# Optimization experiments

Measured on AMD Instinct MI355X. Metric: run time of the kernel, lower is better.

## Reference

```python
import jax, jax.numpy as jnp
import numpy as np

B, N, NC = 16, 25200, 80          # batch, raw predictions, classes (COCO)
CONF_THRES = 0.25
IOU_THRES = 0.45
MAX_CAND = 1000                    # candidates kept after score top-k (pre-NMS)
CLS_OFFSET = 4096.0                # class-wise box offset (non-agnostic NMS trick)
EPS = 1e-7


def setup_inputs() -> dict:
    key = jax.random.key(0)
    # raw head output: [x, y, w, h, obj, cls0..cls79], values in [0,1]
    pred = jax.random.uniform(key, (B, N, 5 + NC), dtype=jnp.float32)
    return {"pred": pred}


def _xywh2xyxy(x):
    xy, wh = x[..., :2], x[..., 2:4]
    return jnp.concatenate([xy - wh * 0.5, xy + wh * 0.5], axis=-1)


def _box_iou(boxes):
    # boxes: [C, 4] xyxy -> pairwise IoU [C, C]
    area = (boxes[:, 2] - boxes[:, 0]) * (boxes[:, 3] - boxes[:, 1])
    lt = jnp.maximum(boxes[:, None, :2], boxes[None, :, :2])
    rb = jnp.minimum(boxes[:, None, 2:], boxes[None, :, 2:])
    wh = jnp.clip(rb - lt, 0.0)
    inter = wh[..., 0] * wh[..., 1]
    return inter / (area[:, None] + area[None, :] - inter + EPS)


def _nms_single(p):
    # p: [N, 5+NC] -> (out [MAX_CAND, 6] xyxy/conf/cls zero-padded, keep [MAX_CAND] bool)
    obj = p[:, 4]
    cls_scores = p[:, 5:] * obj[:, None]          # conf = obj * cls
    conf = jnp.max(cls_scores, axis=-1)
    cls_idx = jnp.argmax(cls_scores, axis=-1)
    valid = (obj > CONF_THRES) & (conf > CONF_THRES)
    score = jnp.where(valid, conf, -1.0)

    # pre-NMS top-k by score (sorted descending) — fixed-shape stand-in for boolean filter
    top_scores, idx = jax.lax.top_k(score, MAX_CAND)
    boxes = _xywh2xyxy(p[idx, :4])                # [C, 4]
    kconf = conf[idx]
    kcls = cls_idx[idx].astype(jnp.float32)
    valid_c = top_scores > 0.0

    # class-offset boxes so different classes never overlap (agnostic=False)
    off_boxes = boxes + kcls[:, None] * CLS_OFFSET
    iou = _box_iou(off_boxes)                     # [C, C]

    ar = jnp.arange(MAX_CAND)

    def body(i, keep):
        sup = keep[i] & (iou[i] > IOU_THRES) & (ar > i)
        return keep & jnp.logical_not(sup)

    keep = jax.lax.fori_loop(0, MAX_CAND, body, valid_c)

    out = jnp.concatenate([boxes, kconf[:, None], kcls[:, None]], axis=-1)  # [C, 6]
    out = jnp.where(keep[:, None], out, 0.0)
    return out, keep


def reference(pred):
    out, keep = jax.vmap(_nms_single)(pred)
    return out, keep
```

## Files before the change

### kernel.cpp

```cpp
#include <hip/hip_runtime.h>
#include <stdint.h>

typedef unsigned int u32;
typedef unsigned long long u64;

#define BATCH 16
#define NANCH 25200
#define NCLS 80
#define ROWF 85
#define MAXC 1000
#define CONF_T 0.25f
#define IOU_T 0.45f
#define EPS_F 1e-7f
#define TILE 64
#define NTILES ((NANCH + TILE - 1) / TILE)

__device__ __forceinline__ float iou_ref(float4 a, float4 b) {
#pragma clang fp contract(off)
  float ai = (a.z - a.x) * (a.w - a.y);
  float aj = (b.z - b.x) * (b.w - b.y);
  float ltx = fmaxf(a.x, b.x), lty = fmaxf(a.y, b.y);
  float rbx = fminf(a.z, b.z), rby = fminf(a.w, b.w);
  float wx = fmaxf(rbx - ltx, 0.0f), wy = fmaxf(rby - lty, 0.0f);
  float inter = wx * wy;
  return inter / (ai + aj - inter + EPS_F);
}

__global__ __launch_bounds__(256) void k1_score(const float* __restrict__ pred,
                                                u64* __restrict__ keys,
                                                u32* __restrict__ hist) {
  __shared__ float srow[TILE * ROWF];
  __shared__ u64 skeys[TILE];
  __shared__ u32 lh[256];
  int tid = threadIdx.x;
  int b = blockIdx.y;
  int t0 = blockIdx.x * TILE;
  int ntile = (t0 + TILE <= NANCH) ? TILE : (NANCH - t0);
  int nf4 = (ntile * ROWF) >> 2;

  lh[tid] = 0;
  const float4* src4 = (const float4*)(pred + ((size_t)b * NANCH + t0) * ROWF);
  float4* smem4 = (float4*)srow;
#pragma unroll
  for (int k = 0; k < 6; ++k) {
    int i = k * 256 + tid;
    if (i < nf4) smem4[i] = src4[i];
  }
  __syncthreads();

  int a = tid >> 2;
  int q = tid & 3;
  float best = -1e30f;
  int bidx = 0;
  float obj = 0.0f;
  if (a < ntile) {
    const float* row = srow + a * ROWF;
    obj = row[4];
    int c0 = q * 20;
#pragma unroll
    for (int c = 0; c < 20; ++c) {
      float s = row[5 + c0 + c] * obj;
      if (s > best) { best = s; bidx = c0 + c; }
    }
  }
#pragma unroll
  for (int off = 1; off < 4; off <<= 1) {
    float ob = __shfl_xor(best, off);
    int oi = __shfl_xor(bidx, off);
    if (ob > best || (ob == best && oi < bidx)) { best = ob; bidx = oi; }
  }
  if (q == 0 && a < ntile) {
    int n = t0 + a;
    bool valid = (obj > CONF_T) && (best > CONF_T);
    u32 hi;
    if (valid) hi = __float_as_uint(best) | 0x80000000u;
    else hi = ((u32)n * 2654435761u) >> 1;
    u32 lo = ((u32)(32767 - n) << 7) | (u32)bidx;
    skeys[a] = ((u64)hi << 32) | lo;
    atomicAdd(&lh[hi >> 24], 1u);
  }
  __syncthreads();
  if (tid < ntile) keys[(size_t)b * NANCH + t0 + tid] = skeys[tid];
  u32 v = lh[tid];
  if (v) atomicAdd(&hist[b * 256 + tid], v);
}

__global__ __launch_bounds__(1024) void k2_select(const float* __restrict__ pred,
                                                  const u64* __restrict__ keys,
                                                  const u32* __restrict__ hist,
                                                  float* __restrict__ selbox,
                                                  float* __restrict__ offbox,
                                                  float* __restrict__ selconf,
                                                  float* __restrict__ selcls,
                                                  u32* __restrict__ selvalid) {
  int b = blockIdx.x;
  int tid = threadIdx.x;
  int wv = tid >> 6, lane = tid & 63;
  __shared__ u32 h4[4096];
  __shared__ u32 wsum[16];
  __shared__ u32 sh_sel;
  __shared__ int sh_rank;
  __shared__ u32 scount;
  __shared__ u64 skey[2048];

  const u64* kb = keys + (size_t)b * NANCH;

  if (tid < 256) h4[tid] = hist[b * 256 + tid];
  __syncthreads();
  if (tid < 64) {
    int l = tid;
    u32 a0 = h4[4 * l], a1 = h4[4 * l + 1], a2 = h4[4 * l + 2], a3 = h4[4 * l + 3];
    u32 lsum = a0 + a1 + a2 + a3;
    u32 suf = lsum;
#pragma unroll
    for (int off = 1; off < 64; off <<= 1) {
      u32 tv = __shfl_down(suf, off);
      if (l + off < 64) suf += tv;
    }
    int rank = MAXC;
    u32 e3 = suf - lsum; u32 i3 = e3 + a3;
    u32 e2 = i3;         u32 i2 = e2 + a2;
    u32 e1 = i2;         u32 i1 = e1 + a1;
    u32 e0 = i1;         u32 i0 = e0 + a0;
    if ((int)i3 >= rank && (int)e3 < rank) { sh_sel = 4u*l+3u; sh_rank = rank-(int)e3; }
    if ((int)i2 >= rank && (int)e2 < rank) { sh_sel = 4u*l+2u; sh_rank = rank-(int)e2; }
    if ((int)i1 >= rank && (int)e1 < rank) { sh_sel = 4u*l+1u; sh_rank = rank-(int)e1; }
    if ((int)i0 >= rank && (int)e0 < rank) { sh_sel = 4u*l+0u; sh_rank = rank-(int)e0; }
  }
  __syncthreads();
  u32 prefix = sh_sel;

#pragma unroll
  for (int r = 0; r < 2; ++r) {
    for (int i = tid; i < 4096; i += 1024) h4[i] = 0;
    __syncthreads();
    int psh = (r == 0) ? 24 : 12;
    int bsh = (r == 0) ? 12 : 0;
    for (int i0 = tid; i0 < NANCH; i0 += 4096) {
      int j1 = i0 + 1024, j2 = i0 + 2048, j3 = i0 + 3072;
      u64 k0 = kb[i0];
      u64 k1v = (j1 < NANCH) ? kb[j1] : 0;
      u64 k2v = (j2 < NANCH) ? kb[j2] : 0;
      u64 k3v = (j3 < NANCH) ? kb[j3] : 0;
      u32 h0 = (u32)(k0 >> 32), h1 = (u32)(k1v >> 32);
      u32 h2 = (u32)(k2v >> 32), h3 = (u32)(k3v >> 32);
      if ((h0 >> psh) == prefix) atomicAdd(&h4[(h0 >> bsh) & 0xFFFu], 1u);
      if (j1 < NANCH && (h1 >> psh) == prefix) atomicAdd(&h4[(h1 >> bsh) & 0xFFFu], 1u);
      if (j2 < NANCH && (h2 >> psh) == prefix) atomicAdd(&h4[(h2 >> bsh) & 0xFFFu], 1u);
      if (j3 < NANCH && (h3 >> psh) == prefix) atomicAdd(&h4[(h3 >> bsh) & 0xFFFu], 1u);
    }
    __syncthreads();
    u32 a0 = h4[4 * tid], a1 = h4[4 * tid + 1], a2 = h4[4 * tid + 2], a3 = h4[4 * tid + 3];
    u32 lsum = a0 + a1 + a2 + a3;
    u32 suf = lsum;
#pragma unroll
    for (int off = 1; off < 64; off <<= 1) {
      u32 tv = __shfl_down(suf, off);
      if (lane + off < 64) suf += tv;
    }
    if (lane == 0) wsum[wv] = suf;
    int rank = sh_rank;
    __syncthreads();
    u32 base = 0;
#pragma unroll
    for (int w2 = 0; w2 < 16; ++w2) if (w2 > wv) base += wsum[w2];
    u32 e3 = base + suf - lsum; u32 i3 = e3 + a3;
    u32 e2 = i3;                u32 i2 = e2 + a2;
    u32 e1 = i2;                u32 i1 = e1 + a1;
    u32 e0 = i1;                u32 i0 = e0 + a0;
    if ((int)i3 >= rank && (int)e3 < rank) { sh_sel = 4u*tid+3u; sh_rank = rank-(int)e3; }
    if ((int)i2 >= rank && (int)e2 < rank) { sh_sel = 4u*tid+2u; sh_rank = rank-(int)e2; }
    if ((int)i1 >= rank && (int)e1 < rank) { sh_sel = 4u*tid+1u; sh_rank = rank-(int)e1; }
    if ((int)i0 >= rank && (int)e0 < rank) { sh_sel = 4u*tid+0u; sh_rank = rank-(int)e0; }
    __syncthreads();
    prefix = (prefix << 12) | sh_sel;
  }
  u32 Cstar = prefix;

  if (tid == 0) scount = 0;
  skey[tid] = ~0ull;
  skey[tid + 1024] = ~0ull;
  __syncthreads();
  for (int i0 = tid; i0 < NANCH; i0 += 4096) {
    int j1 = i0 + 1024, j2 = i0 + 2048, j3 = i0 + 3072;
    u64 k0 = kb[i0];
    u64 k1v = (j1 < NANCH) ? kb[j1] : 0;
    u64 k2v = (j2 < NANCH) ? kb[j2] : 0;
    u64 k3v = (j3 < NANCH) ? kb[j3] : 0;
    if ((u32)(k0 >> 32) >= Cstar) { u32 p = atomicAdd(&scount, 1u); if (p < 2048) skey[p] = ~k0; }
    if (j1 < NANCH && (u32)(k1v >> 32) >= Cstar) { u32 p = atomicAdd(&scount, 1u); if (p < 2048) skey[p] = ~k1v; }
    if (j2 < NANCH && (u32)(k2v >> 32) >= Cstar) { u32 p = atomicAdd(&scount, 1u); if (p < 2048) skey[p] = ~k2v; }
    if (j3 < NANCH && (u32)(k3v >> 32) >= Cstar) { u32 p = atomicAdd(&scount, 1u); if (p < 2048) skey[p] = ~k3v; }
  }
  __syncthreads();
  for (u32 kk = 2; kk <= 2048; kk <<= 1) {
    for (u32 j = kk >> 1; j > 0; j >>= 1) {
      for (int idx = tid; idx < 2048; idx += 1024) {
        u32 ixj = (u32)idx ^ j;
        if (ixj > (u32)idx) {
          u64 a = skey[idx], c2 = skey[ixj];
          bool up = ((idx & kk) == 0);
          if (up ? (a > c2) : (a < c2)) { skey[idx] = c2; skey[ixj] = a; }
        }
      }
      __syncthreads();
    }
  }
  if (tid < MAXC) {
    u64 k = ~skey[tid];
    u32 hi = (u32)(k >> 32);
    u32 lo = (u32)k;
    u32 n = 32767u - (lo >> 7);
    u32 ci = lo & 127u;
    bool valid = hi > 0x80000000u;
    float conf = valid ? __uint_as_float(hi & 0x7FFFFFFFu) : 0.0f;
    const float* pr = pred + ((size_t)b * NANCH + n) * ROWF;
    float x = pr[0], y = pr[1], w = pr[2], h2 = pr[3];
    float x1 = x - w * 0.5f, y1 = y - h2 * 0.5f;
    float x2 = x + w * 0.5f, y2 = y + h2 * 0.5f;
    float cf = (float)ci;
    float off = cf * 4096.0f;
    int o = b * MAXC + tid;
    ((float4*)selbox)[o] = make_float4(x1, y1, x2, y2);
    ((float4*)offbox)[o] = make_float4(x1 + off, y1 + off, x2 + off, y2 + off);
    selconf[o] = conf;
    selcls[o] = cf;
    selvalid[o] = valid ? 1u : 0u;
  }
}

__global__ __launch_bounds__(256) void k3_dt(const float4* __restrict__ offbox4,
                                             u64* __restrict__ dt) {
  int wid = blockIdx.x * 4 + (threadIdx.x >> 6);
  int lane = threadIdx.x & 63;
  int b = wid / MAXC;
  int i = wid % MAXC;
  float4 bi = offbox4[b * MAXC + i];
  u64 myword = 0;
  for (int w = 0; w < 16; ++w) {
    int j = w * 64 + lane;
    int jc = (j < MAXC) ? j : 0;
    float4 bj = offbox4[b * MAXC + jc];
    float iou = iou_ref(bi, bj);
    bool bit = (iou > IOU_T) && (j < i);
    u64 bal = __ballot(bit ? 1 : 0);
    if (lane == w) myword = bal;
  }
  if (lane < 16) dt[((size_t)b * 16 + lane) * MAXC + i] = myword;
}

__global__ __launch_bounds__(1024) void k4_jacobi(const u64* __restrict__ dt,
                                                  const u32* __restrict__ selvalid,
                                                  const float* __restrict__ selbox,
                                                  const float* __restrict__ selconf,
                                                  const float* __restrict__ selcls,
                                                  float* __restrict__ out) {
  int b = blockIdx.x;
  int tid = threadIdx.x;
  int wv = tid >> 6, lane = tid & 63;
  __shared__ u64 keepv[16];
  __shared__ u32 changed;
  bool valid = false;
  u64 dtr[16];
  if (tid < MAXC) {
    valid = selvalid[b * MAXC + tid] != 0u;
#pragma unroll
    for (int w = 0; w < 16; ++w) dtr[w] = dt[((size_t)b * 16 + w) * MAXC + tid];
  } else {
#pragma unroll
    for (int w = 0; w < 16; ++w) dtr[w] = 0ull;
  }
  u64 bal0 = __ballot(valid ? 1 : 0);
  if (tid == 0) changed = 0;
  if (lane == 0) keepv[wv] = bal0;
  __syncthreads();
  for (int pass = 0; pass < MAXC; ++pass) {
    u64 kv[16];
#pragma unroll
    for (int w = 0; w < 16; ++w) kv[w] = keepv[w];
    u64 s = 0;
#pragma unroll
    for (int w = 0; w < 16; ++w) s |= dtr[w] & kv[w];
    bool nk = valid && (s == 0ull);
    u64 bal = __ballot(nk ? 1 : 0);
    __syncthreads();
    if (lane == 0 && bal != kv[wv]) { keepv[wv] = bal; atomicOr(&changed, 1u); }
    __syncthreads();
    u32 ch = changed;
    __syncthreads();
    if (tid == 0) changed = 0;
    if (!ch) break;
  }
  if (tid < MAXC) {
    bool kept = ((keepv[wv] >> lane) & 1ull) != 0ull;
    size_t o = (size_t)b * MAXC + tid;
    const float4* sb4 = (const float4*)selbox;
    float4 bx = sb4[o];
    float cf = selconf[o], cl = selcls[o];
    float* orow = out + o * 6;
    orow[0] = kept ? bx.x : 0.0f;
    orow[1] = kept ? bx.y : 0.0f;
    orow[2] = kept ? bx.z : 0.0f;
    orow[3] = kept ? bx.w : 0.0f;
    orow[4] = kept ? cf : 0.0f;
    orow[5] = kept ? cl : 0.0f;
    out[(size_t)BATCH * MAXC * 6 + o] = kept ? 1.0f : 0.0f;
  }
}

extern "C" void kernel_launch(void* const* d_in, const int* in_sizes, int n_in,
                              void* d_out, int out_size, void* d_ws, size_t ws_size,
                              hipStream_t stream) {
  const float* pred = (const float*)d_in[0];
  float* out = (float*)d_out;
  char* ws = (char*)d_ws;
  size_t off = 0;
  auto alloc = [&](size_t bytes) -> void* {
    void* p = ws + off;
    off = (off + bytes + 255) & ~(size_t)255;
    return p;
  };
  u64* keys     = (u64*)alloc((size_t)BATCH * NANCH * 8);
  u32* hist     = (u32*)alloc((size_t)BATCH * 256 * 4);
  float* selbox = (float*)alloc((size_t)BATCH * MAXC * 4 * 4);
  float* offbox = (float*)alloc((size_t)BATCH * MAXC * 4 * 4);
  float* selconf= (float*)alloc((size_t)BATCH * MAXC * 4);
  float* selcls = (float*)alloc((size_t)BATCH * MAXC * 4);
  u32* selvalid = (u32*)alloc((size_t)BATCH * MAXC * 4);
  u64* dt       = (u64*)alloc(((size_t)BATCH * 16 * MAXC + 1024) * 8);
  (void)ws_size; (void)in_sizes; (void)n_in; (void)out_size;

  hipMemsetAsync(hist, 0, (size_t)BATCH * 256 * 4, stream);

  dim3 g1(NTILES, BATCH);
  k1_score<<<g1, 256, 0, stream>>>(pred, keys, hist);
  k2_select<<<BATCH, 1024, 0, stream>>>(pred, keys, hist, selbox, offbox,
                                        selconf, selcls, selvalid);
  k3_dt<<<(BATCH * MAXC) / 4, 256, 0, stream>>>((const float4*)offbox, dt);
  k4_jacobi<<<BATCH, 1024, 0, stream>>>(dt, selvalid, selbox, selconf,
                                        selcls, out);
}
```

Baseline: 275.5 us.

## Fuse all NMS stages into one cooperative persistent kernel with grid syncs

Replaces the four separate launches and the histogram memset with a single cooperative kernel of 256 blocks of 1024 threads, separated by grid.sync barriers. The global histogram atomics in the scoring stage are dropped, and the selection stage instead builds its own 12/12/8-bit radix histograms directly from the keys. The scoring tile grows to 128 anchors with 8 threads per anchor. The aim is to remove launch gaps and global atomics, at the cost of grid-wide barriers and mostly idle blocks during the per-batch phases; a non-cooperative fallback path is kept.

```diff
diff --git a/kernel.cpp b/kernel.cpp
--- a/kernel.cpp
+++ b/kernel.cpp
@@ -1,5 +1,8 @@
 #include <hip/hip_runtime.h>
+#include <hip/hip_cooperative_groups.h>
 #include <stdint.h>
+
+namespace cg = cooperative_groups;
 
 typedef unsigned int u32;
 typedef unsigned long long u64;
@@ -12,8 +15,9 @@
 #define CONF_T 0.25f
 #define IOU_T 0.45f
 #define EPS_F 1e-7f
-#define TILE 64
-#define NTILES ((NANCH + TILE - 1) / TILE)
+#define TILE2 128
+#define TPB2 ((NANCH + TILE2 - 1) / TILE2)
+#define NTILE2TOT (BATCH * TPB2)
 
 __device__ __forceinline__ float iou_ref(float4 a, float4 b) {
 #pragma clang fp contract(off)
@@ -26,45 +30,37 @@
   return inter / (ai + aj - inter + EPS_F);
 }
 
-__global__ __launch_bounds__(256) void k1_score(const float* __restrict__ pred,
-                                                u64* __restrict__ keys,
-                                                u32* __restrict__ hist) {
-  __shared__ float srow[TILE * ROWF];
-  __shared__ u64 skeys[TILE];
-  __shared__ u32 lh[256];
-  int tid = threadIdx.x;
-  int b = blockIdx.y;
-  int t0 = blockIdx.x * TILE;
-  int ntile = (t0 + TILE <= NANCH) ? TILE : (NANCH - t0);
+__device__ __forceinline__ void phase1_tile(const float* __restrict__ pred,
+                                            u64* __restrict__ keys,
+                                            int tile, int tid,
+                                            float* srow, u64* skeys2) {
+  int b = tile / TPB2;
+  int ti = tile % TPB2;
+  int t0 = ti * TILE2;
+  int ntile = (t0 + TILE2 <= NANCH) ? TILE2 : (NANCH - t0);
   int nf4 = (ntile * ROWF) >> 2;
-
-  lh[tid] = 0;
   const float4* src4 = (const float4*)(pred + ((size_t)b * NANCH + t0) * ROWF);
   float4* smem4 = (float4*)srow;
-#pragma unroll
-  for (int k = 0; k < 6; ++k) {
-    int i = k * 256 + tid;
-    if (i < nf4) smem4[i] = src4[i];
-  }
-  __syncthreads();
-
-  int a = tid >> 2;
-  int q = tid & 3;
+  __syncthreads();
+  for (int i = tid; i < nf4; i += 1024) smem4[i] = src4[i];
+  __syncthreads();
+  int a = tid >> 3;
+  int q = tid & 7;
   float best = -1e30f;
   int bidx = 0;
   float obj = 0.0f;
   if (a < ntile) {
     const float* row = srow + a * ROWF;
     obj = row[4];
-    int c0 = q * 20;
-#pragma unroll
-    for (int c = 0; c < 20; ++c) {
+    int c0 = q * 10;
+#pragma unroll
+    for (int c = 0; c < 10; ++c) {
       float s = row[5 + c0 + c] * obj;
       if (s > best) { best = s; bidx = c0 + c; }
     }
   }
 #pragma unroll
-  for (int off = 1; off < 4; off <<= 1) {
+  for (int off = 1; off < 8; off <<= 1) {
     float ob = __shfl_xor(best, off);
     int oi = __shfl_xor(bidx, off);
     if (ob > best || (ob == best && oi < bidx)) { best = ob; bidx = oi; }
@@ -72,70 +68,32 @@
   if (q == 0 && a < ntile) {
     int n = t0 + a;
     bool valid = (obj > CONF_T) && (best > CONF_T);
-    u32 hi;
-    if (valid) hi = __float_as_uint(best) | 0x80000000u;
-    else hi = ((u32)n * 2654435761u) >> 1;
+    u32 hi = valid ? (__float_as_uint(best) | 0x80000000u)
+                   : (((u32)n * 2654435761u) >> 1);
     u32 lo = ((u32)(32767 - n) << 7) | (u32)bidx;
-    skeys[a] = ((u64)hi << 32) | lo;
-    atomicAdd(&lh[hi >> 24], 1u);
-  }
-  __syncthreads();
-  if (tid < ntile) keys[(size_t)b * NANCH + t0 + tid] = skeys[tid];
-  u32 v = lh[tid];
-  if (v) atomicAdd(&hist[b * 256 + tid], v);
-}
-
-__global__ __launch_bounds__(1024) void k2_select(const float* __restrict__ pred,
-                                                  const u64* __restrict__ keys,
-                                                  const u32* __restrict__ hist,
-                                                  float* __restrict__ selbox,
-                                                  float* __restrict__ offbox,
-                                                  float* __restrict__ selconf,
-                                                  float* __restrict__ selcls,
-                                                  u32* __restrict__ selvalid) {
-  int b = blockIdx.x;
-  int tid = threadIdx.x;
+    skeys2[a] = ((u64)hi << 32) | lo;
+  }
+  __syncthreads();
+  if (tid < ntile) keys[(size_t)b * NANCH + t0 + tid] = skeys2[tid];
+}
+
+__device__ __forceinline__ void phase2_impl(const float* __restrict__ pred,
+                                            const u64* __restrict__ keys,
+                                            float* __restrict__ selbox,
+                                            float* __restrict__ offbox,
+                                            float* __restrict__ selconf,
+                                            float* __restrict__ selcls,
+                                            u32* __restrict__ selvalid,
+                                            int b, int tid,
+                                            u32* h4, u64* skey, u32* wsum,
+                                            u32* sh_sel, int* sh_rank,
+                                            u32* scount) {
   int wv = tid >> 6, lane = tid & 63;
-  __shared__ u32 h4[4096];
-  __shared__ u32 wsum[16];
-  __shared__ u32 sh_sel;
-  __shared__ int sh_rank;
-  __shared__ u32 scount;
-  __shared__ u64 skey[2048];
-
   const u64* kb = keys + (size_t)b * NANCH;
-
-  if (tid < 256) h4[tid] = hist[b * 256 + tid];
-  __syncthreads();
-  if (tid < 64) {
-    int l = tid;
-    u32 a0 = h4[4 * l], a1 = h4[4 * l + 1], a2 = h4[4 * l + 2], a3 = h4[4 * l + 3];
-    u32 lsum = a0 + a1 + a2 + a3;
-    u32 suf = lsum;
-#pragma unroll
-    for (int off = 1; off < 64; off <<= 1) {
-      u32 tv = __shfl_down(suf, off);
-      if (l + off < 64) suf += tv;
-    }
-    int rank = MAXC;
-    u32 e3 = suf - lsum; u32 i3 = e3 + a3;
-    u32 e2 = i3;         u32 i2 = e2 + a2;
-    u32 e1 = i2;         u32 i1 = e1 + a1;
-    u32 e0 = i1;         u32 i0 = e0 + a0;
-    if ((int)i3 >= rank && (int)e3 < rank) { sh_sel = 4u*l+3u; sh_rank = rank-(int)e3; }
-    if ((int)i2 >= rank && (int)e2 < rank) { sh_sel = 4u*l+2u; sh_rank = rank-(int)e2; }
-    if ((int)i1 >= rank && (int)e1 < rank) { sh_sel = 4u*l+1u; sh_rank = rank-(int)e1; }
-    if ((int)i0 >= rank && (int)e0 < rank) { sh_sel = 4u*l+0u; sh_rank = rank-(int)e0; }
-  }
-  __syncthreads();
-  u32 prefix = sh_sel;
-
-#pragma unroll
+  u32 prefix = 0;
   for (int r = 0; r < 2; ++r) {
     for (int i = tid; i < 4096; i += 1024) h4[i] = 0;
     __syncthreads();
-    int psh = (r == 0) ? 24 : 12;
-    int bsh = (r == 0) ? 12 : 0;
     for (int i0 = tid; i0 < NANCH; i0 += 4096) {
       int j1 = i0 + 1024, j2 = i0 + 2048, j3 = i0 + 3072;
       u64 k0 = kb[i0];
@@ -144,10 +102,17 @@
       u64 k3v = (j3 < NANCH) ? kb[j3] : 0;
       u32 h0 = (u32)(k0 >> 32), h1 = (u32)(k1v >> 32);
       u32 h2 = (u32)(k2v >> 32), h3 = (u32)(k3v >> 32);
-      if ((h0 >> psh) == prefix) atomicAdd(&h4[(h0 >> bsh) & 0xFFFu], 1u);
-      if (j1 < NANCH && (h1 >> psh) == prefix) atomicAdd(&h4[(h1 >> bsh) & 0xFFFu], 1u);
-      if (j2 < NANCH && (h2 >> psh) == prefix) atomicAdd(&h4[(h2 >> bsh) & 0xFFFu], 1u);
-      if (j3 < NANCH && (h3 >> psh) == prefix) atomicAdd(&h4[(h3 >> bsh) & 0xFFFu], 1u);
+      if (r == 0) {
+        atomicAdd(&h4[h0 >> 20], 1u);
+        if (j1 < NANCH) atomicAdd(&h4[h1 >> 20], 1u);
+        if (j2 < NANCH) atomicAdd(&h4[h2 >> 20], 1u);
+        if (j3 < NANCH) atomicAdd(&h4[h3 >> 20], 1u);
+      } else {
+        if ((h0 >> 20) == prefix) atomicAdd(&h4[(h0 >> 8) & 0xFFFu], 1u);
+        if (j1 < NANCH && (h1 >> 20) == prefix) atomicAdd(&h4[(h1 >> 8) & 0xFFFu], 1u);
+        if (j2 < NANCH && (h2 >> 20) == prefix) atomicAdd(&h4[(h2 >> 8) & 0xFFFu], 1u);
+        if (j3 < NANCH && (h3 >> 20) == prefix) atomicAdd(&h4[(h3 >> 8) & 0xFFFu], 1u);
+      }
     }
     __syncthreads();
     u32 a0 = h4[4 * tid], a1 = h4[4 * tid + 1], a2 = h4[4 * tid + 2], a3 = h4[4 * tid + 3];
@@ -159,27 +124,23 @@
       if (lane + off < 64) suf += tv;
     }
     if (lane == 0) wsum[wv] = suf;
-    int rank = sh_rank;
+    int rank = (r == 0) ? MAXC : *sh_rank;
     __syncthreads();
     u32 base = 0;
 #pragma unroll
     for (int w2 = 0; w2 < 16; ++w2) if (w2 > wv) base += wsum[w2];
-    u32 e3 = base + suf - lsum; u32 i3 = e3 + a3;
-    u32 e2 = i3;                u32 i2 = e2 + a2;
-    u32 e1 = i2;                u32 i1 = e1 + a1;
-    u32 e0 = i1;                u32 i0 = e0 + a0;
-    if ((int)i3 >= rank && (int)e3 < rank) { sh_sel = 4u*tid+3u; sh_rank = rank-(int)e3; }
-    if ((int)i2 >= rank && (int)e2 < rank) { sh_sel = 4u*tid+2u; sh_rank = rank-(int)e2; }
-    if ((int)i1 >= rank && (int)e1 < rank) { sh_sel = 4u*tid+1u; sh_rank = rank-(int)e1; }
-    if ((int)i0 >= rank && (int)e0 < rank) { sh_sel = 4u*tid+0u; sh_rank = rank-(int)e0; }
-    __syncthreads();
-    prefix = (prefix << 12) | sh_sel;
-  }
-  u32 Cstar = prefix;
-
-  if (tid == 0) scount = 0;
-  skey[tid] = ~0ull;
-  skey[tid + 1024] = ~0ull;
+    u32 e3 = base + suf - lsum; u32 i3v = e3 + a3;
+    u32 e2 = i3v;               u32 i2v = e2 + a2;
+    u32 e1 = i2v;               u32 i1v = e1 + a1;
+    u32 e0 = i1v;               u32 i0v = e0 + a0;
+    if ((int)i3v >= rank && (int)e3 < rank) { *sh_sel = 4u*tid+3u; *sh_rank = rank-(int)e3; }
+    if ((int)i2v >= rank && (int)e2 < rank) { *sh_sel = 4u*tid+2u; *sh_rank = rank-(int)e2; }
+    if ((int)i1v >= rank && (int)e1 < rank) { *sh_sel = 4u*tid+1u; *sh_rank = rank-(int)e1; }
+    if ((int)i0v >= rank && (int)e0 < rank) { *sh_sel = 4u*tid+0u; *sh_rank = rank-(int)e0; }
+    __syncthreads();
+    prefix = (prefix << 12) | *sh_sel;
+  }
+  if (tid < 256) h4[tid] = 0;
   __syncthreads();
   for (int i0 = tid; i0 < NANCH; i0 += 4096) {
     int j1 = i0 + 1024, j2 = i0 + 2048, j3 = i0 + 3072;
@@ -187,10 +148,51 @@
     u64 k1v = (j1 < NANCH) ? kb[j1] : 0;
     u64 k2v = (j2 < NANCH) ? kb[j2] : 0;
     u64 k3v = (j3 < NANCH) ? kb[j3] : 0;
-    if ((u32)(k0 >> 32) >= Cstar) { u32 p = atomicAdd(&scount, 1u); if (p < 2048) skey[p] = ~k0; }
-    if (j1 < NANCH && (u32)(k1v >> 32) >= Cstar) { u32 p = atomicAdd(&scount, 1u); if (p < 2048) skey[p] = ~k1v; }
-    if (j2 < NANCH && (u32)(k2v >> 32) >= Cstar) { u32 p = atomicAdd(&scount, 1u); if (p < 2048) skey[p] = ~k2v; }
-    if (j3 < NANCH && (u32)(k3v >> 32) >= Cstar) { u32 p = atomicAdd(&scount, 1u); if (p < 2048) skey[p] = ~k3v; }
+    u32 h0 = (u32)(k0 >> 32), h1 = (u32)(k1v >> 32);
+    u32 h2 = (u32)(k2v >> 32), h3 = (u32)(k3v >> 32);
+    if ((h0 >> 8) == prefix) atomicAdd(&h4[h0 & 0xFFu], 1u);
+    if (j1 < NANCH && (h1 >> 8) == prefix) atomicAdd(&h4[h1 & 0xFFu], 1u);
+    if (j2 < NANCH && (h2 >> 8) == prefix) atomicAdd(&h4[h2 & 0xFFu], 1u);
+    if (j3 < NANCH && (h3 >> 8) == prefix) atomicAdd(&h4[h3 & 0xFFu], 1u);
+  }
+  __syncthreads();
+  if (tid < 64) {
+    int l = tid;
+    u32 a0 = h4[4 * l], a1 = h4[4 * l + 1], a2 = h4[4 * l + 2], a3 = h4[4 * l + 3];
+    u32 lsum = a0 + a1 + a2 + a3;
+    u32 suf = lsum;
+#pragma unroll
+    for (int off = 1; off < 64; off <<= 1) {
+      u32 tv = __shfl_down(suf, off);
+      if (l + off < 64) suf += tv;
+    }
+    int rank = *sh_rank;
+    u32 e3 = suf - lsum; u32 i3v = e3 + a3;
+    u32 e2 = i3v;        u32 i2v = e2 + a2;
+    u32 e1 = i2v;        u32 i1v = e1 + a1;
+    u32 e0 = i1v;        u32 i0v = e0 + a0;
+    if ((int)i3v >= rank && (int)e3 < rank) { *sh_sel = 4u*l+3u; }
+    if ((int)i2v >= rank && (int)e2 < rank) { *sh_sel = 4u*l+2u; }
+    if ((int)i1v >= rank && (int)e1 < rank) { *sh_sel = 4u*l+1u; }
+    if ((int)i0v >= rank && (int)e0 < rank) { *sh_sel = 4u*l+0u; }
+  }
+  __syncthreads();
+  u32 Cstar = (prefix << 8) | *sh_sel;
+
+  if (tid == 0) *scount = 0;
+  skey[tid] = ~0ull;
+  skey[tid + 1024] = ~0ull;
+  __syncthreads();
+  for (int i0 = tid; i0 < NANCH; i0 += 4096) {
+    int j1 = i0 + 1024, j2 = i0 + 2048, j3 = i0 + 3072;
+    u64 k0 = kb[i0];
+    u64 k1v = (j1 < NANCH) ? kb[j1] : 0;
+    u64 k2v = (j2 < NANCH) ? kb[j2] : 0;
+    u64 k3v = (j3 < NANCH) ? kb[j3] : 0;
+    if ((u32)(k0 >> 32) >= Cstar) { u32 p = atomicAdd(scount, 1u); if (p < 2048) skey[p] = ~k0; }
+    if (j1 < NANCH && (u32)(k1v >> 32) >= Cstar) { u32 p = atomicAdd(scount, 1u); if (p < 2048) skey[p] = ~k1v; }
+    if (j2 < NANCH && (u32)(k2v >> 32) >= Cstar) { u32 p = atomicAdd(scount, 1u); if (p < 2048) skey[p] = ~k2v; }
+    if (j3 < NANCH && (u32)(k3v >> 32) >= Cstar) { u32 p = atomicAdd(scount, 1u); if (p < 2048) skey[p] = ~k3v; }
   }
   __syncthreads();
   for (u32 kk = 2; kk <= 2048; kk <<= 1) {
@@ -229,12 +231,11 @@
   }
 }
 
-__global__ __launch_bounds__(256) void k3_dt(const float4* __restrict__ offbox4,
-                                             u64* __restrict__ dt) {
-  int wid = blockIdx.x * 4 + (threadIdx.x >> 6);
-  int lane = threadIdx.x & 63;
-  int b = wid / MAXC;
-  int i = wid % MAXC;
+__device__ __forceinline__ void phase3_row(const float4* __restrict__ offbox4,
+                                           u64* __restrict__ dt,
+                                           int row, int lane) {
+  int b = row / MAXC;
+  int i = row % MAXC;
   float4 bi = offbox4[b * MAXC + i];
   u64 myword = 0;
   for (int w = 0; w < 16; ++w) {
@@ -249,17 +250,15 @@
   if (lane < 16) dt[((size_t)b * 16 + lane) * MAXC + i] = myword;
 }
 
-__global__ __launch_bounds__(1024) void k4_jacobi(const u64* __restrict__ dt,
-                                                  const u32* __restrict__ selvalid,
-                                                  const float* __restrict__ selbox,
-                                                  const float* __restrict__ selconf,
-                                                  const float* __restrict__ selcls,
-                                                  float* __restrict__ out) {
-  int b = blockIdx.x;
-  int tid = threadIdx.x;
+__device__ __forceinline__ void phase4_impl(const u64* __restrict__ dt,
+                                            const u32* __restrict__ selvalid,
+                                            const float* __restrict__ selbox,
+                                            const float* __restrict__ selconf,
+                                            const float* __restrict__ selcls,
+                                            float* __restrict__ out,
+                                            int b, int tid,
+                                            u64* keepv, u32* changed) {
   int wv = tid >> 6, lane = tid & 63;
-  __shared__ u64 keepv[16];
-  __shared__ u32 changed;
   bool valid = false;
   u64 dtr[16];
   if (tid < MAXC) {
@@ -271,7 +270,7 @@
     for (int w = 0; w < 16; ++w) dtr[w] = 0ull;
   }
   u64 bal0 = __ballot(valid ? 1 : 0);
-  if (tid == 0) changed = 0;
+  if (tid == 0) *changed = 0;
   if (lane == 0) keepv[wv] = bal0;
   __syncthreads();
   for (int pass = 0; pass < MAXC; ++pass) {
@@ -284,18 +283,17 @@
     bool nk = valid && (s == 0ull);
     u64 bal = __ballot(nk ? 1 : 0);
     __syncthreads();
-    if (lane == 0 && bal != kv[wv]) { keepv[wv] = bal; atomicOr(&changed, 1u); }
-    __syncthreads();
-    u32 ch = changed;
-    __syncthreads();
-    if (tid == 0) changed = 0;
+    if (lane == 0 && bal != kv[wv]) { keepv[wv] = bal; atomicOr(changed, 1u); }
+    __syncthreads();
+    u32 ch = *changed;
+    __syncthreads();
+    if (tid == 0) *changed = 0;
     if (!ch) break;
   }
   if (tid < MAXC) {
     bool kept = ((keepv[wv] >> lane) & 1ull) != 0ull;
     size_t o = (size_t)b * MAXC + tid;
-    const float4* sb4 = (const float4*)selbox;
-    float4 bx = sb4[o];
+    float4 bx = ((const float4*)selbox)[o];
     float cf = selconf[o], cl = selcls[o];
     float* orow = out + o * 6;
     orow[0] = kept ? bx.x : 0.0f;
@@ -306,6 +304,85 @@
     orow[5] = kept ? cl : 0.0f;
     out[(size_t)BATCH * MAXC * 6 + o] = kept ? 1.0f : 0.0f;
   }
+}
+
+__global__ __launch_bounds__(1024) void fused_all(const float* __restrict__ pred,
+                                                  u64* __restrict__ keys,
+                                                  float* __restrict__ selbox,
+                                                  float* __restrict__ offbox,
+                                                  float* __restrict__ selconf,
+                                                  float* __restrict__ selcls,
+                                                  u32* __restrict__ selvalid,
+                                                  u64* __restrict__ dt,
+                                                  float* __restrict__ out) {
+  cg::grid_group grid = cg::this_grid();
+  __shared__ __align__(16) float srow[TILE2 * ROWF];
+  __shared__ u64 skeys2[TILE2];
+  __shared__ u32 wsum[16];
+  __shared__ u32 sh_sel; __shared__ int sh_rank; __shared__ u32 scount;
+  __shared__ u64 keepv[16]; __shared__ u32 changed;
+  int tid = threadIdx.x, bid = blockIdx.x;
+  int lane = tid & 63;
+
+  for (int tile = bid; tile < NTILE2TOT; tile += 256)
+    phase1_tile(pred, keys, tile, tid, srow, skeys2);
+  __threadfence();
+  grid.sync();
+
+  if (bid < BATCH) {
+    u32* h4 = (u32*)srow;
+    u64* skey = (u64*)(srow + 4096);
+    phase2_impl(pred, keys, selbox, offbox, selconf, selcls, selvalid,
+                bid, tid, h4, skey, wsum, &sh_sel, &sh_rank, &scount);
+  }
+  __threadfence();
+  grid.sync();
+
+  int gw = bid * 16 + (tid >> 6);
+  for (int row = gw; row < BATCH * MAXC; row += 4096)
+    phase3_row((const float4*)offbox, dt, row, lane);
+  __threadfence();
+  grid.sync();
+
+  if (bid < BATCH)
+    phase4_impl(dt, selvalid, selbox, selconf, selcls, out, bid, tid,
+                keepv, &changed);
+}
+
+__global__ __launch_bounds__(1024) void k1f(const float* __restrict__ pred,
+                                            u64* __restrict__ keys) {
+  __shared__ __align__(16) float srow[TILE2 * ROWF];
+  __shared__ u64 skeys2[TILE2];
+  phase1_tile(pred, keys, blockIdx.x, threadIdx.x, srow, skeys2);
+}
+__global__ __launch_bounds__(1024) void k2f(const float* __restrict__ pred,
+                                            const u64* __restrict__ keys,
+                                            float* __restrict__ selbox,
+                                            float* __restrict__ offbox,
+                                            float* __restrict__ selconf,
+                                            float* __restrict__ selcls,
+                                            u32* __restrict__ selvalid) {
+  __shared__ __align__(16) u32 h4[4096];
+  __shared__ u64 skey[2048];
+  __shared__ u32 wsum[16];
+  __shared__ u32 sh_sel; __shared__ int sh_rank; __shared__ u32 scount;
+  phase2_impl(pred, keys, selbox, offbox, selconf, selcls, selvalid,
+              blockIdx.x, threadIdx.x, h4, skey, wsum, &sh_sel, &sh_rank, &scount);
+}
+__global__ __launch_bounds__(256) void k3f(const float4* __restrict__ offbox4,
+                                           u64* __restrict__ dt) {
+  int row = blockIdx.x * 4 + (threadIdx.x >> 6);
+  phase3_row(offbox4, dt, row, threadIdx.x & 63);
+}
+__global__ __launch_bounds__(1024) void k4f(const u64* __restrict__ dt,
+                                            const u32* __restrict__ selvalid,
+                                            const float* __restrict__ selbox,
+                                            const float* __restrict__ selconf,
+                                            const float* __restrict__ selcls,
+                                            float* __restrict__ out) {
+  __shared__ u64 keepv[16]; __shared__ u32 changed;
+  phase4_impl(dt, selvalid, selbox, selconf, selcls, out,
+              blockIdx.x, threadIdx.x, keepv, &changed);
 }
 
 extern "C" void kernel_launch(void* const* d_in, const int* in_sizes, int n_in,
@@ -321,22 +398,26 @@
     return p;
   };
   u64* keys     = (u64*)alloc((size_t)BATCH * NANCH * 8);
-  u32* hist     = (u32*)alloc((size_t)BATCH * 256 * 4);
   float* selbox = (float*)alloc((size_t)BATCH * MAXC * 4 * 4);
   float* offbox = (float*)alloc((size_t)BATCH * MAXC * 4 * 4);
   float* selconf= (float*)alloc((size_t)BATCH * MAXC * 4);
   float* selcls = (float*)alloc((size_t)BATCH * MAXC * 4);
   u32* selvalid = (u32*)alloc((size_t)BATCH * MAXC * 4);
-  u64* dt       = (u64*)alloc(((size_t)BATCH * 16 * MAXC + 1024) * 8);
+  u64* dt       = (u64*)alloc((size_t)BATCH * 16 * MAXC * 8);
   (void)ws_size; (void)in_sizes; (void)n_in; (void)out_size;
 
-  hipMemsetAsync(hist, 0, (size_t)BATCH * 256 * 4, stream);
-
-  dim3 g1(NTILES, BATCH);
-  k1_score<<<g1, 256, 0, stream>>>(pred, keys, hist);
-  k2_select<<<BATCH, 1024, 0, stream>>>(pred, keys, hist, selbox, offbox,
-                                        selconf, selcls, selvalid);
-  k3_dt<<<(BATCH * MAXC) / 4, 256, 0, stream>>>((const float4*)offbox, dt);
-  k4_jacobi<<<BATCH, 1024, 0, stream>>>(dt, selvalid, selbox, selconf,
-                                        selcls, out);
-}
+  void* args[] = {(void*)&pred, (void*)&keys, (void*)&selbox, (void*)&offbox,
+                  (void*)&selconf, (void*)&selcls, (void*)&selvalid,
+                  (void*)&dt, (void*)&out};
+  hipError_t rc = hipLaunchCooperativeKernel((const void*)fused_all,
+                                             dim3(256), dim3(1024),
+                                             args, 0, stream);
+  if (rc != hipSuccess) {
+    k1f<<<NTILE2TOT, 1024, 0, stream>>>(pred, keys);
+    k2f<<<BATCH, 1024, 0, stream>>>(pred, keys, selbox, offbox,
+                                    selconf, selcls, selvalid);
+    k3f<<<(BATCH * MAXC) / 4, 256, 0, stream>>>((const float4*)offbox, dt);
+    k4f<<<BATCH, 1024, 0, stream>>>(dt, selvalid, selbox, selconf,
+                                    selcls, out);
+  }
+}
```

Measured after the change: 611.4 us. 122% more time.
